# Performance work log

Measured on AMD Instinct MI355X. Metric: run time of the kernel, lower is better.

Reference implementation:

```python
import jax, jax.numpy as jnp
import numpy as np

D_MODEL = 1024
N_HEADS = 16
HEAD_DIM = D_MODEL // N_HEADS
ROPE_BASE = 10000.0


def setup_inputs() -> dict:
    key = jax.random.key(0)
    ks = jax.random.split(key, 9)
    s = 0.02
    inp = {
        "x": jax.random.normal(ks[0], (2, 2048, D_MODEL), dtype=jnp.float32),
        "Wq": jax.random.normal(ks[1], (D_MODEL, D_MODEL), dtype=jnp.float32) * s,
        "bq": jnp.zeros((D_MODEL,), dtype=jnp.float32),
        "Wk": jax.random.normal(ks[2], (D_MODEL, D_MODEL), dtype=jnp.float32) * s,
        "bk": jnp.zeros((D_MODEL,), dtype=jnp.float32),
        "Wv": jax.random.normal(ks[3], (D_MODEL, D_MODEL), dtype=jnp.float32) * s,
        "bv": jnp.zeros((D_MODEL,), dtype=jnp.float32),
        "Wo": jax.random.normal(ks[4], (D_MODEL, D_MODEL), dtype=jnp.float32) * s,
        "bo": jnp.zeros((D_MODEL,), dtype=jnp.float32),
    }
    return inp


def _rope_cos_sin(T, head_dim, dtype):
    inv_freq = 1.0 / (ROPE_BASE ** (jnp.arange(0, head_dim, 2, dtype=jnp.float32) / head_dim))
    pos = jnp.arange(T, dtype=jnp.float32)
    freqs = jnp.outer(pos, inv_freq)              # [T, head_dim/2]
    emb = jnp.concatenate([freqs, freqs], axis=-1)  # [T, head_dim]
    return jnp.cos(emb).astype(dtype), jnp.sin(emb).astype(dtype)


def _rotate_half(x):
    x1, x2 = jnp.split(x, 2, axis=-1)
    return jnp.concatenate([-x2, x1], axis=-1)


def reference(x, Wq, bq, Wk, bk, Wv, bv, Wo, bo):
    B, T, _ = x.shape
    H, Dh = N_HEADS, HEAD_DIM
    # projections (torch Linear: x @ W.T + b)
    q = (x @ Wq.T + bq).reshape(B, T, H, Dh).transpose(0, 2, 1, 3)  # [B,H,T,Dh]
    k = (x @ Wk.T + bk).reshape(B, T, H, Dh).transpose(0, 2, 1, 3)
    v = (x @ Wv.T + bv).reshape(B, T, H, Dh).transpose(0, 2, 1, 3)
    cos, sin = _rope_cos_sin(T, Dh, x.dtype)  # [T, Dh]
    cos = cos[None, None]
    sin = sin[None, None]
    q = q * cos + _rotate_half(q) * sin
    k = k * cos + _rotate_half(k) * sin
    scale = 1.0 / jnp.sqrt(jnp.asarray(Dh, dtype=x.dtype))
    attn = jnp.einsum("bhqd,bhkd->bhqk", q, k) * scale
    attn = jax.nn.softmax(attn, axis=-1)
    out = jnp.einsum("bhqk,bhkd->bhqd", attn, v)  # [B,H,T,Dh]
    out = out.transpose(0, 2, 1, 3).reshape(B, T, H * Dh)
    return out @ Wo.T + bo
```

## Files before the change

### kernel.cpp

```cpp
#include <hip/hip_runtime.h>
#include <hip/hip_bf16.h>
#include <cstdint>

#define D_MODEL 1024
#define NHEADS 16
#define HDIM 64
#define SEQ 2048
#define NBATCH 2
#define BT (NBATCH * SEQ)

typedef short bf16x8 __attribute__((ext_vector_type(8)));
typedef float f32x4 __attribute__((ext_vector_type(4)));
typedef unsigned short u16;

__device__ inline u16 f2bf(float f) {
    union { float f; unsigned int u; } x;
    x.f = f;
    unsigned int r = (x.u + 0x7fffu + ((x.u >> 16) & 1u)) >> 16;
    return (u16)r;
}

__device__ inline u16 f2bf_fast(float f) {
    union { float f; unsigned int u; } x;
    x.f = f;
    return (u16)((x.u + 0x8000u) >> 16);
}

__device__ inline void async_copy16(const u16* g, u16* l) {
    __builtin_amdgcn_global_load_lds((const __attribute__((address_space(1))) void*)g,
                                     (__attribute__((address_space(3))) void*)l, 16, 0, 0);
}

__global__ void cast_x_kernel(const float* __restrict__ src, u16* __restrict__ dst, int n4) {
    int i = blockIdx.x * blockDim.x + threadIdx.x;
    if (i >= n4) return;
    float4 v = ((const float4*)src)[i];
    ushort4 o;
    o.x = f2bf(v.x); o.y = f2bf(v.y); o.z = f2bf(v.z); o.w = f2bf(v.w);
    ((ushort4*)dst)[i] = o;
}

__global__ void cast_w_kernel(const float* __restrict__ wq, const float* __restrict__ wk,
                              const float* __restrict__ wv, const float* __restrict__ wo,
                              u16* __restrict__ dq, u16* __restrict__ dk,
                              u16* __restrict__ dv, u16* __restrict__ dow) {
    int z = blockIdx.z;
    const float* s = (z == 0) ? wq : (z == 1) ? wk : (z == 2) ? wv : wo;
    u16* d = (z == 0) ? dq : (z == 1) ? dk : (z == 2) ? dv : dow;
    int i = blockIdx.x * blockDim.x + threadIdx.x;
    float4 v = ((const float4*)s)[i];
    ushort4 o;
    o.x = f2bf(v.x); o.y = f2bf(v.y); o.z = f2bf(v.z); o.w = f2bf(v.w);
    ((ushort4*)d)[i] = o;
}

__global__ void rope_table_kernel(float* __restrict__ cosT, float* __restrict__ sinT) {
    int t = blockIdx.x;
    int d = threadIdx.x;
    float invf = expf(-(float)(d & 31) * (9.210340371976184f / 32.0f));
    float ang = (float)t * invf;
    float s, c;
    sincosf(ang, &s, &c);
    cosT[t * HDIM + d] = c;
    sinT[t * HDIM + d] = s;
}

__device__ inline void gemm_tile_core(const u16* __restrict__ A, const u16* __restrict__ Bw,
                                      int blkM, int blkN,
                                      u16* Asmem, u16* Bsmem, f32x4 acc[4][4]) {
    const int tid = threadIdx.x;
    const int lane = tid & 63;
    const int wave = tid >> 6;
    const int waveM = wave >> 1, waveN = wave & 1;
    const int quad = lane >> 4, l16 = lane & 15;

    const int srow = tid >> 2;
    const int scol = (tid & 3) << 3;
    const u16* Ag0 = A + (size_t)(blkM * 128 + srow) * D_MODEL + scol;
    const u16* Ag1 = Ag0 + (size_t)64 * D_MODEL;
    const u16* Bg0 = Bw + (size_t)(blkN * 128 + srow) * D_MODEL + scol;
    const u16* Bg1 = Bg0 + (size_t)64 * D_MODEL;
    u16* Al0 = Asmem + srow * 32 + scol;
    u16* Al1 = Al0 + 64 * 32;
    u16* Bl0 = Bsmem + srow * 32 + scol;
    u16* Bl1 = Bl0 + 64 * 32;

    for (int k0 = 0; k0 < D_MODEL; k0 += 32) {
        __syncthreads();
        async_copy16(Ag0 + k0, Al0);
        async_copy16(Ag1 + k0, Al1);
        async_copy16(Bg0 + k0, Bl0);
        async_copy16(Bg1 + k0, Bl1);
        __syncthreads();
        bf16x8 af[4], bfr[4];
#pragma unroll
        for (int mt = 0; mt < 4; ++mt)
            af[mt] = *(const bf16x8*)&Asmem[(waveM * 64 + mt * 16 + l16) * 32 + quad * 8];
#pragma unroll
        for (int nt = 0; nt < 4; ++nt)
            bfr[nt] = *(const bf16x8*)&Bsmem[(waveN * 64 + nt * 16 + l16) * 32 + quad * 8];
#pragma unroll
        for (int mt = 0; mt < 4; ++mt)
#pragma unroll
            for (int nt = 0; nt < 4; ++nt)
                acc[mt][nt] = __builtin_amdgcn_mfma_f32_16x16x32_bf16(af[mt], bfr[nt], acc[mt][nt], 0, 0, 0);
    }
}

#define QSCALE 0.1803368801111204f

__global__ __launch_bounds__(256) void gemm_qkv_kernel(
    const u16* __restrict__ xb,
    const u16* __restrict__ wqb, const u16* __restrict__ wkb, const u16* __restrict__ wvb,
    const float* __restrict__ bq, const float* __restrict__ bk, const float* __restrict__ bv,
    const float* __restrict__ cosT, const float* __restrict__ sinT,
    u16* __restrict__ Qb, u16* __restrict__ Kb, u16* __restrict__ VTb) {
    __shared__ __align__(16) u16 Asmem[128 * 32];
    __shared__ __align__(16) u16 Bsmem[128 * 32];
    const int z = blockIdx.z;
    const u16* Bw = (z == 0) ? wqb : (z == 1) ? wkb : wvb;
    const float* bias = (z == 0) ? bq : (z == 1) ? bk : bv;

    f32x4 acc[4][4];
#pragma unroll
    for (int mt = 0; mt < 4; ++mt)
#pragma unroll
        for (int nt = 0; nt < 4; ++nt)
            acc[mt][nt] = (f32x4){0.f, 0.f, 0.f, 0.f};

    gemm_tile_core(xb, Bw, blockIdx.x, blockIdx.y, Asmem, Bsmem, acc);

    const int lane = threadIdx.x & 63, wave = threadIdx.x >> 6;
    const int waveM = wave >> 1, waveN = wave & 1;
    const int quad = lane >> 4, l16 = lane & 15;
    const int gm0 = blockIdx.x * 128 + waveM * 64 + quad * 4;
    const int gn0 = blockIdx.y * 128 + waveN * 64 + l16;

    float bvv[4];
#pragma unroll
    for (int nt = 0; nt < 4; ++nt) bvv[nt] = bias[gn0 + nt * 16];
#pragma unroll
    for (int mt = 0; mt < 4; ++mt)
#pragma unroll
        for (int nt = 0; nt < 4; ++nt)
#pragma unroll
            for (int r = 0; r < 4; ++r) acc[mt][nt][r] += bvv[nt];

    if (z < 2) {
        u16* dst = (z == 0) ? Qb : Kb;
        const float post = (z == 0) ? QSCALE : 1.0f;
#pragma unroll
        for (int mt = 0; mt < 4; ++mt) {
#pragma unroll
            for (int nt = 0; nt < 4; ++nt) {
                int n = gn0 + nt * 16;
                int d = n & 63, h = n >> 6;
#pragma unroll
                for (int r = 0; r < 4; ++r) {
                    int gm = gm0 + mt * 16 + r;
                    int t = gm & (SEQ - 1), b = gm >> 11;
                    float c = cosT[t * HDIM + d], s = sinT[t * HDIM + d];
                    float part = acc[mt][nt ^ 2][r];
                    float rot = (d < 32) ? -part : part;
                    float val = (acc[mt][nt][r] * c + rot * s) * post;
                    dst[((b * NHEADS + h) * SEQ + t) * HDIM + d] = f2bf(val);
                }
            }
        }
    } else {
#pragma unroll
        for (int mt = 0; mt < 4; ++mt) {
#pragma unroll
            for (int nt = 0; nt < 4; ++nt) {
                int n = gn0 + nt * 16;
                int d = n & 63, h = n >> 6;
#pragma unroll
                for (int r = 0; r < 4; ++r) {
                    int gm = gm0 + mt * 16 + r;
                    int t = gm & (SEQ - 1), b = gm >> 11;
                    VTb[((b * NHEADS + h) * HDIM + d) * SEQ + t] = f2bf(acc[mt][nt][r]);
                }
            }
        }
    }
}

#define LPAD 72

__global__ __launch_bounds__(256) void flash_kernel(
    const u16* __restrict__ Qb, const u16* __restrict__ Kb, const u16* __restrict__ VTb,
    u16* __restrict__ attn) {
    __shared__ __align__(16) u16 Ks[64 * LPAD];
    __shared__ __align__(16) u16 VTs[64 * LPAD];
    __shared__ __align__(16) u16 Ps[4][16 * LPAD];

    const int tid = threadIdx.x;
    const int wave = tid >> 6, lane = tid & 63;
    const int quad = lane >> 4, l16 = lane & 15;
    const int bh = blockIdx.y;
    const u16* Qh = Qb + (size_t)bh * SEQ * HDIM;
    const u16* Kh = Kb + (size_t)bh * SEQ * HDIM;
    const u16* Vh = VTb + (size_t)bh * HDIM * SEQ;
    const int qbase = blockIdx.x * 64 + wave * 16;

    bf16x8 aq[2];
#pragma unroll
    for (int ks = 0; ks < 2; ++ks)
        aq[ks] = *(const bf16x8*)&Qh[(qbase + l16) * HDIM + ks * 32 + quad * 8];

    f32x4 o[4];
    float lsum[4] = {0.f, 0.f, 0.f, 0.f};
#pragma unroll
    for (int nt = 0; nt < 4; ++nt) o[nt] = (f32x4){0.f, 0.f, 0.f, 0.f};

    const int lr = tid >> 3, lc = (tid & 7) * 8;

    for (int kt = 0; kt < SEQ / 64; ++kt) {
        __syncthreads();
        *(int4*)&Ks[lr * LPAD + lc] = *(const int4*)&Kh[(kt * 64 + lr) * HDIM + lc];
        *(int4*)&Ks[(lr + 32) * LPAD + lc] = *(const int4*)&Kh[(kt * 64 + lr + 32) * HDIM + lc];
        *(int4*)&VTs[lr * LPAD + lc] = *(const int4*)&Vh[lr * SEQ + kt * 64 + lc];
        *(int4*)&VTs[(lr + 32) * LPAD + lc] = *(const int4*)&Vh[(lr + 32) * SEQ + kt * 64 + lc];
        __syncthreads();

        f32x4 sacc[4];
#pragma unroll
        for (int nt = 0; nt < 4; ++nt) sacc[nt] = (f32x4){0.f, 0.f, 0.f, 0.f};
#pragma unroll
        for (int ks = 0; ks < 2; ++ks) {
            bf16x8 bk_[4];
#pragma unroll
            for (int nt = 0; nt < 4; ++nt)
                bk_[nt] = *(const bf16x8*)&Ks[(nt * 16 + l16) * LPAD + ks * 32 + quad * 8];
#pragma unroll
            for (int nt = 0; nt < 4; ++nt)
                sacc[nt] = __builtin_amdgcn_mfma_f32_16x16x32_bf16(aq[ks], bk_[nt], sacc[nt], 0, 0, 0);
        }

#pragma unroll
        for (int nt = 0; nt < 4; ++nt) {
#pragma unroll
            for (int r = 0; r < 4; ++r) {
                float p = __builtin_amdgcn_exp2f(fminf(sacc[nt][r], 60.0f));
                lsum[r] += p;
                Ps[wave][(quad * 4 + r) * LPAD + nt * 16 + l16] = f2bf_fast(p);
            }
        }

#pragma unroll
        for (int ks = 0; ks < 2; ++ks) {
            bf16x8 ap, bv_[4];
            ap = *(const bf16x8*)&Ps[wave][l16 * LPAD + ks * 32 + quad * 8];
#pragma unroll
            for (int nt = 0; nt < 4; ++nt)
                bv_[nt] = *(const bf16x8*)&VTs[(nt * 16 + l16) * LPAD + ks * 32 + quad * 8];
#pragma unroll
            for (int nt = 0; nt < 4; ++nt)
                o[nt] = __builtin_amdgcn_mfma_f32_16x16x32_bf16(ap, bv_[nt], o[nt], 0, 0, 0);
        }
    }

#pragma unroll
    for (int off = 1; off < 16; off <<= 1)
#pragma unroll
        for (int r = 0; r < 4; ++r)
            lsum[r] += __shfl_xor(lsum[r], off, 64);

    const int b = bh >> 4, h = bh & 15;
    float rinv[4];
#pragma unroll
    for (int r = 0; r < 4; ++r) rinv[r] = 1.0f / lsum[r];
#pragma unroll
    for (int nt = 0; nt < 4; ++nt) {
        int d = nt * 16 + l16;
#pragma unroll
        for (int r = 0; r < 4; ++r) {
            int q = qbase + quad * 4 + r;
            attn[((size_t)(b * SEQ + q)) * D_MODEL + h * HDIM + d] = f2bf(o[nt][r] * rinv[r]);
        }
    }
}

__global__ __launch_bounds__(256) void gemm_out_kernel(
    const u16* __restrict__ attn, const u16* __restrict__ wob,
    const float* __restrict__ bo, float* __restrict__ dout) {
    __shared__ __align__(16) u16 Asmem[128 * 32];
    __shared__ __align__(16) u16 Bsmem[128 * 32];

    f32x4 acc[4][4];
#pragma unroll
    for (int mt = 0; mt < 4; ++mt)
#pragma unroll
        for (int nt = 0; nt < 4; ++nt) acc[mt][nt] = (f32x4){0.f, 0.f, 0.f, 0.f};

    gemm_tile_core(attn, wob, blockIdx.x, blockIdx.y, Asmem, Bsmem, acc);

    const int lane = threadIdx.x & 63, wave = threadIdx.x >> 6;
    const int waveM = wave >> 1, waveN = wave & 1;
    const int quad = lane >> 4, l16 = lane & 15;
    const int gm0 = blockIdx.x * 128 + waveM * 64 + quad * 4;
    const int gn0 = blockIdx.y * 128 + waveN * 64 + l16;

    float bvv[4];
#pragma unroll
    for (int nt = 0; nt < 4; ++nt) bvv[nt] = bo[gn0 + nt * 16];
#pragma unroll
    for (int mt = 0; mt < 4; ++mt)
#pragma unroll
        for (int nt = 0; nt < 4; ++nt)
#pragma unroll
            for (int r = 0; r < 4; ++r)
                dout[(size_t)(gm0 + mt * 16 + r) * D_MODEL + gn0 + nt * 16] = acc[mt][nt][r] + bvv[nt];
}

extern "C" void kernel_launch(void* const* d_in, const int* in_sizes, int n_in,
                              void* d_out, int out_size, void* d_ws, size_t ws_size,
                              hipStream_t stream) {
    const float* x  = (const float*)d_in[0];
    const float* Wq = (const float*)d_in[1];
    const float* bq = (const float*)d_in[2];
    const float* Wk = (const float*)d_in[3];
    const float* bk = (const float*)d_in[4];
    const float* Wv = (const float*)d_in[5];
    const float* bv = (const float*)d_in[6];
    const float* Wo = (const float*)d_in[7];
    const float* bo = (const float*)d_in[8];
    float* dout = (float*)d_out;

    char* ws = (char*)d_ws;
    size_t off = 0;
    u16* xb  = (u16*)(ws + off); off += (size_t)BT * D_MODEL * 2;
    u16* wqb = (u16*)(ws + off); off += (size_t)D_MODEL * D_MODEL * 2;
    u16* wkb = (u16*)(ws + off); off += (size_t)D_MODEL * D_MODEL * 2;
    u16* wvb = (u16*)(ws + off); off += (size_t)D_MODEL * D_MODEL * 2;
    u16* wob = (u16*)(ws + off); off += (size_t)D_MODEL * D_MODEL * 2;
    u16* Qb  = (u16*)(ws + off); off += (size_t)BT * D_MODEL * 2;
    u16* Kb  = (u16*)(ws + off); off += (size_t)BT * D_MODEL * 2;
    u16* VTb = (u16*)(ws + off); off += (size_t)BT * D_MODEL * 2;
    u16* attn = (u16*)(ws + off); off += (size_t)BT * D_MODEL * 2;
    float* cosT = (float*)(ws + off); off += (size_t)SEQ * HDIM * 4;
    float* sinT = (float*)(ws + off); off += (size_t)SEQ * HDIM * 4;

    cast_x_kernel<<<dim3((BT * D_MODEL / 4 + 255) / 256), 256, 0, stream>>>(x, xb, BT * D_MODEL / 4);
    cast_w_kernel<<<dim3(D_MODEL * D_MODEL / 4 / 256, 1, 4), 256, 0, stream>>>(Wq, Wk, Wv, Wo, wqb, wkb, wvb, wob);
    rope_table_kernel<<<dim3(SEQ), dim3(HDIM), 0, stream>>>(cosT, sinT);
    gemm_qkv_kernel<<<dim3(BT / 128, D_MODEL / 128, 3), 256, 0, stream>>>(
        xb, wqb, wkb, wvb, bq, bk, bv, cosT, sinT, Qb, Kb, VTb);
    flash_kernel<<<dim3(SEQ / 64, NBATCH * NHEADS), 256, 0, stream>>>(Qb, Kb, VTb, attn);
    gemm_out_kernel<<<dim3(BT / 128, D_MODEL / 128), 256, 0, stream>>>(attn, wob, bo, dout);
}
```

Measured before the change: 242.8 us.

## Double queries per wave in flash attention, fuse prep kernels, vectorize V^T stores

The flash kernel now handles 128 queries per block, with 32 per wave, so each K/V tile loaded into LDS is reused across twice as many queries. S is computed transposed (K as the A operand), which lets P be written to LDS as packed 8-byte stores and shrinks the row-sum reduction. The three preprocessing kernels (casts and RoPE table) are merged into one launch, and the RoPE table computes each half once and writes it to both halves. The V^T epilogue in the QKV GEMM writes four packed bf16 values per store instead of scalar stores. In exchange the flash grid has half as many blocks, and register pressure per wave rises.

```diff
diff --git a/kernel.cpp b/kernel.cpp
--- a/kernel.cpp
+++ b/kernel.cpp
@@ -12,18 +12,19 @@
 typedef short bf16x8 __attribute__((ext_vector_type(8)));
 typedef float f32x4 __attribute__((ext_vector_type(4)));
 typedef unsigned short u16;
+typedef unsigned int u32;
 
 __device__ inline u16 f2bf(float f) {
-    union { float f; unsigned int u; } x;
+    union { float f; u32 u; } x;
     x.f = f;
-    unsigned int r = (x.u + 0x7fffu + ((x.u >> 16) & 1u)) >> 16;
+    u32 r = (x.u + 0x7fffu + ((x.u >> 16) & 1u)) >> 16;
     return (u16)r;
 }
 
-__device__ inline u16 f2bf_fast(float f) {
-    union { float f; unsigned int u; } x;
-    x.f = f;
-    return (u16)((x.u + 0x8000u) >> 16);
+__device__ inline u32 pack2bf(float a, float b) {
+    union { float f; u32 u; } x, y;
+    x.f = a; y.f = b;
+    return ((x.u + 0x8000u) >> 16) | ((y.u + 0x8000u) & 0xffff0000u);
 }
 
 __device__ inline void async_copy16(const u16* g, u16* l) {
@@ -31,38 +32,44 @@
                                      (__attribute__((address_space(3))) void*)l, 16, 0, 0);
 }
 
-__global__ void cast_x_kernel(const float* __restrict__ src, u16* __restrict__ dst, int n4) {
-    int i = blockIdx.x * blockDim.x + threadIdx.x;
-    if (i >= n4) return;
-    float4 v = ((const float4*)src)[i];
-    ushort4 o;
-    o.x = f2bf(v.x); o.y = f2bf(v.y); o.z = f2bf(v.z); o.w = f2bf(v.w);
-    ((ushort4*)dst)[i] = o;
-}
-
-__global__ void cast_w_kernel(const float* __restrict__ wq, const float* __restrict__ wk,
-                              const float* __restrict__ wv, const float* __restrict__ wo,
-                              u16* __restrict__ dq, u16* __restrict__ dk,
-                              u16* __restrict__ dv, u16* __restrict__ dow) {
-    int z = blockIdx.z;
-    const float* s = (z == 0) ? wq : (z == 1) ? wk : (z == 2) ? wv : wo;
-    u16* d = (z == 0) ? dq : (z == 1) ? dk : (z == 2) ? dv : dow;
-    int i = blockIdx.x * blockDim.x + threadIdx.x;
-    float4 v = ((const float4*)s)[i];
-    ushort4 o;
-    o.x = f2bf(v.x); o.y = f2bf(v.y); o.z = f2bf(v.z); o.w = f2bf(v.w);
-    ((ushort4*)d)[i] = o;
-}
-
-__global__ void rope_table_kernel(float* __restrict__ cosT, float* __restrict__ sinT) {
-    int t = blockIdx.x;
-    int d = threadIdx.x;
-    float invf = expf(-(float)(d & 31) * (9.210340371976184f / 32.0f));
-    float ang = (float)t * invf;
-    float s, c;
-    sincosf(ang, &s, &c);
-    cosT[t * HDIM + d] = c;
-    sinT[t * HDIM + d] = s;
+#define X4 (BT * D_MODEL / 4)
+#define W4 (D_MODEL * D_MODEL / 4)
+#define ROPE_N (SEQ * 32)
+
+__global__ void prep_kernel(const float* __restrict__ x,
+                            const float* __restrict__ wq, const float* __restrict__ wk,
+                            const float* __restrict__ wv, const float* __restrict__ wo,
+                            u16* __restrict__ xb,
+                            u16* __restrict__ dq, u16* __restrict__ dk,
+                            u16* __restrict__ dv, u16* __restrict__ dow,
+                            float* __restrict__ cosT, float* __restrict__ sinT) {
+    int idx = blockIdx.x * blockDim.x + threadIdx.x;
+    if (idx < X4) {
+        float4 v = ((const float4*)x)[idx];
+        ushort4 o;
+        o.x = f2bf(v.x); o.y = f2bf(v.y); o.z = f2bf(v.z); o.w = f2bf(v.w);
+        ((ushort4*)xb)[idx] = o;
+    } else if (idx < X4 + 4 * W4) {
+        int j = idx - X4;
+        int w = j >> 18, i = j & (W4 - 1);
+        const float* s = (w == 0) ? wq : (w == 1) ? wk : (w == 2) ? wv : wo;
+        u16* d = (w == 0) ? dq : (w == 1) ? dk : (w == 2) ? dv : dow;
+        float4 v = ((const float4*)s)[i];
+        ushort4 o;
+        o.x = f2bf(v.x); o.y = f2bf(v.y); o.z = f2bf(v.z); o.w = f2bf(v.w);
+        ((ushort4*)d)[i] = o;
+    } else {
+        int j = idx - (X4 + 4 * W4);
+        if (j < ROPE_N) {
+            int t = j >> 5, dd = j & 31;
+            float invf = exp2f(-(float)dd * (13.287712379549449f / 32.0f));
+            float ang = (float)t * invf;
+            float s, c;
+            sincosf(ang, &s, &c);
+            cosT[t * HDIM + dd] = c;      cosT[t * HDIM + dd + 32] = c;
+            sinT[t * HDIM + dd] = s;      sinT[t * HDIM + dd + 32] = s;
+        }
+    }
 }
 
 __device__ inline void gemm_tile_core(const u16* __restrict__ A, const u16* __restrict__ Bw,
@@ -170,16 +177,16 @@
     } else {
 #pragma unroll
         for (int mt = 0; mt < 4; ++mt) {
+            int gm = gm0 + mt * 16;
+            int t0 = gm & (SEQ - 1), b = gm >> 11;
 #pragma unroll
             for (int nt = 0; nt < 4; ++nt) {
                 int n = gn0 + nt * 16;
                 int d = n & 63, h = n >> 6;
-#pragma unroll
-                for (int r = 0; r < 4; ++r) {
-                    int gm = gm0 + mt * 16 + r;
-                    int t = gm & (SEQ - 1), b = gm >> 11;
-                    VTb[((b * NHEADS + h) * HDIM + d) * SEQ + t] = f2bf(acc[mt][nt][r]);
-                }
+                uint2 w;
+                w.x = pack2bf(acc[mt][nt][0], acc[mt][nt][1]);
+                w.y = pack2bf(acc[mt][nt][2], acc[mt][nt][3]);
+                *(uint2*)&VTb[((size_t)(b * NHEADS + h) * HDIM + d) * SEQ + t0] = w;
             }
         }
     }
@@ -192,7 +199,7 @@
     u16* __restrict__ attn) {
     __shared__ __align__(16) u16 Ks[64 * LPAD];
     __shared__ __align__(16) u16 VTs[64 * LPAD];
-    __shared__ __align__(16) u16 Ps[4][16 * LPAD];
+    __shared__ __align__(16) u16 Ps[4][32 * LPAD];
 
     const int tid = threadIdx.x;
     const int wave = tid >> 6, lane = tid & 63;
@@ -201,82 +208,108 @@
     const u16* Qh = Qb + (size_t)bh * SEQ * HDIM;
     const u16* Kh = Kb + (size_t)bh * SEQ * HDIM;
     const u16* Vh = VTb + (size_t)bh * HDIM * SEQ;
-    const int qbase = blockIdx.x * 64 + wave * 16;
-
-    bf16x8 aq[2];
-#pragma unroll
-    for (int ks = 0; ks < 2; ++ks)
-        aq[ks] = *(const bf16x8*)&Qh[(qbase + l16) * HDIM + ks * 32 + quad * 8];
-
-    f32x4 o[4];
-    float lsum[4] = {0.f, 0.f, 0.f, 0.f};
-#pragma unroll
-    for (int nt = 0; nt < 4; ++nt) o[nt] = (f32x4){0.f, 0.f, 0.f, 0.f};
-
-    const int lr = tid >> 3, lc = (tid & 7) * 8;
+    const int qblk = blockIdx.x * 128 + wave * 32;
+    u16* Pw = (u16*)Ps[wave];
+
+    bf16x8 aq[2][2];
+#pragma unroll
+    for (int nt2 = 0; nt2 < 2; ++nt2)
+#pragma unroll
+        for (int ks = 0; ks < 2; ++ks)
+            aq[nt2][ks] = *(const bf16x8*)&Qh[(qblk + nt2 * 16 + l16) * HDIM + ks * 32 + quad * 8];
+
+    f32x4 o[2][4];
+    float lsum[2] = {0.f, 0.f};
+#pragma unroll
+    for (int mt2 = 0; mt2 < 2; ++mt2)
+#pragma unroll
+        for (int nt = 0; nt < 4; ++nt) o[mt2][nt] = (f32x4){0.f, 0.f, 0.f, 0.f};
+
+    const int lr = tid >> 2;
+    const int lc = (tid & 3) * 16;
 
     for (int kt = 0; kt < SEQ / 64; ++kt) {
         __syncthreads();
         *(int4*)&Ks[lr * LPAD + lc] = *(const int4*)&Kh[(kt * 64 + lr) * HDIM + lc];
-        *(int4*)&Ks[(lr + 32) * LPAD + lc] = *(const int4*)&Kh[(kt * 64 + lr + 32) * HDIM + lc];
+        *(int4*)&Ks[lr * LPAD + lc + 8] = *(const int4*)&Kh[(kt * 64 + lr) * HDIM + lc + 8];
         *(int4*)&VTs[lr * LPAD + lc] = *(const int4*)&Vh[lr * SEQ + kt * 64 + lc];
-        *(int4*)&VTs[(lr + 32) * LPAD + lc] = *(const int4*)&Vh[(lr + 32) * SEQ + kt * 64 + lc];
+        *(int4*)&VTs[lr * LPAD + lc + 8] = *(const int4*)&Vh[lr * SEQ + kt * 64 + lc + 8];
         __syncthreads();
 
-        f32x4 sacc[4];
-#pragma unroll
-        for (int nt = 0; nt < 4; ++nt) sacc[nt] = (f32x4){0.f, 0.f, 0.f, 0.f};
+        f32x4 sacc[4][2];
+#pragma unroll
+        for (int mt = 0; mt < 4; ++mt)
+#pragma unroll
+            for (int nt2 = 0; nt2 < 2; ++nt2) sacc[mt][nt2] = (f32x4){0.f, 0.f, 0.f, 0.f};
 #pragma unroll
         for (int ks = 0; ks < 2; ++ks) {
-            bf16x8 bk_[4];
+            bf16x8 kf[4];
+#pragma unroll
+            for (int mt = 0; mt < 4; ++mt)
+                kf[mt] = *(const bf16x8*)&Ks[(mt * 16 + l16) * LPAD + ks * 32 + quad * 8];
+#pragma unroll
+            for (int mt = 0; mt < 4; ++mt)
+#pragma unroll
+                for (int nt2 = 0; nt2 < 2; ++nt2)
+                    sacc[mt][nt2] = __builtin_amdgcn_mfma_f32_16x16x32_bf16(kf[mt], aq[nt2][ks], sacc[mt][nt2], 0, 0, 0);
+        }
+
+#pragma unroll
+        for (int mt = 0; mt < 4; ++mt) {
+#pragma unroll
+            for (int nt2 = 0; nt2 < 2; ++nt2) {
+                float p0 = __builtin_amdgcn_exp2f(fminf(sacc[mt][nt2][0], 60.0f));
+                float p1 = __builtin_amdgcn_exp2f(fminf(sacc[mt][nt2][1], 60.0f));
+                float p2 = __builtin_amdgcn_exp2f(fminf(sacc[mt][nt2][2], 60.0f));
+                float p3 = __builtin_amdgcn_exp2f(fminf(sacc[mt][nt2][3], 60.0f));
+                lsum[nt2] += (p0 + p1) + (p2 + p3);
+                uint2 w;
+                w.x = pack2bf(p0, p1);
+                w.y = pack2bf(p2, p3);
+                *(uint2*)&Pw[(nt2 * 16 + l16) * LPAD + mt * 16 + quad * 4] = w;
+            }
+        }
+
+#pragma unroll
+        for (int ks = 0; ks < 2; ++ks) {
+            bf16x8 pf[2], vf[4];
+#pragma unroll
+            for (int mt2 = 0; mt2 < 2; ++mt2)
+                pf[mt2] = *(const bf16x8*)&Pw[(mt2 * 16 + l16) * LPAD + ks * 32 + quad * 8];
 #pragma unroll
             for (int nt = 0; nt < 4; ++nt)
-                bk_[nt] = *(const bf16x8*)&Ks[(nt * 16 + l16) * LPAD + ks * 32 + quad * 8];
-#pragma unroll
-            for (int nt = 0; nt < 4; ++nt)
-                sacc[nt] = __builtin_amdgcn_mfma_f32_16x16x32_bf16(aq[ks], bk_[nt], sacc[nt], 0, 0, 0);
-        }
-
+                vf[nt] = *(const bf16x8*)&VTs[(nt * 16 + l16) * LPAD + ks * 32 + quad * 8];
+#pragma unroll
+            for (int mt2 = 0; mt2 < 2; ++mt2)
+#pragma unroll
+                for (int nt = 0; nt < 4; ++nt)
+                    o[mt2][nt] = __builtin_amdgcn_mfma_f32_16x16x32_bf16(pf[mt2], vf[nt], o[mt2][nt], 0, 0, 0);
+        }
+    }
+
+#pragma unroll
+    for (int nt2 = 0; nt2 < 2; ++nt2) {
+        lsum[nt2] += __shfl_xor(lsum[nt2], 16, 64);
+        lsum[nt2] += __shfl_xor(lsum[nt2], 32, 64);
+    }
+    float rinv[2][4];
+#pragma unroll
+    for (int mt2 = 0; mt2 < 2; ++mt2)
+#pragma unroll
+        for (int r = 0; r < 4; ++r)
+            rinv[mt2][r] = 1.0f / __shfl(lsum[mt2], quad * 4 + r, 64);
+
+    const int b = bh >> 4, h = bh & 15;
+#pragma unroll
+    for (int mt2 = 0; mt2 < 2; ++mt2) {
 #pragma unroll
         for (int nt = 0; nt < 4; ++nt) {
+            int d = nt * 16 + l16;
 #pragma unroll
             for (int r = 0; r < 4; ++r) {
-                float p = __builtin_amdgcn_exp2f(fminf(sacc[nt][r], 60.0f));
-                lsum[r] += p;
-                Ps[wave][(quad * 4 + r) * LPAD + nt * 16 + l16] = f2bf_fast(p);
+                int q = qblk + mt2 * 16 + quad * 4 + r;
+                attn[((size_t)(b * SEQ + q)) * D_MODEL + h * HDIM + d] = f2bf(o[mt2][nt][r] * rinv[mt2][r]);
             }
-        }
-
-#pragma unroll
-        for (int ks = 0; ks < 2; ++ks) {
-            bf16x8 ap, bv_[4];
-            ap = *(const bf16x8*)&Ps[wave][l16 * LPAD + ks * 32 + quad * 8];
-#pragma unroll
-            for (int nt = 0; nt < 4; ++nt)
-                bv_[nt] = *(const bf16x8*)&VTs[(nt * 16 + l16) * LPAD + ks * 32 + quad * 8];
-#pragma unroll
-            for (int nt = 0; nt < 4; ++nt)
-                o[nt] = __builtin_amdgcn_mfma_f32_16x16x32_bf16(ap, bv_[nt], o[nt], 0, 0, 0);
-        }
-    }
-
-#pragma unroll
-    for (int off = 1; off < 16; off <<= 1)
-#pragma unroll
-        for (int r = 0; r < 4; ++r)
-            lsum[r] += __shfl_xor(lsum[r], off, 64);
-
-    const int b = bh >> 4, h = bh & 15;
-    float rinv[4];
-#pragma unroll
-    for (int r = 0; r < 4; ++r) rinv[r] = 1.0f / lsum[r];
-#pragma unroll
-    for (int nt = 0; nt < 4; ++nt) {
-        int d = nt * 16 + l16;
-#pragma unroll
-        for (int r = 0; r < 4; ++r) {
-            int q = qbase + quad * 4 + r;
-            attn[((size_t)(b * SEQ + q)) * D_MODEL + h * HDIM + d] = f2bf(o[nt][r] * rinv[r]);
         }
     }
 }
@@ -341,11 +374,11 @@
     float* cosT = (float*)(ws + off); off += (size_t)SEQ * HDIM * 4;
     float* sinT = (float*)(ws + off); off += (size_t)SEQ * HDIM * 4;
 
-    cast_x_kernel<<<dim3((BT * D_MODEL / 4 + 255) / 256), 256, 0, stream>>>(x, xb, BT * D_MODEL / 4);
-    cast_w_kernel<<<dim3(D_MODEL * D_MODEL / 4 / 256, 1, 4), 256, 0, stream>>>(Wq, Wk, Wv, Wo, wqb, wkb, wvb, wob);
-    rope_table_kernel<<<dim3(SEQ), dim3(HDIM), 0, stream>>>(cosT, sinT);
+    const int prepN = X4 + 4 * W4 + ROPE_N;
+    prep_kernel<<<dim3((prepN + 255) / 256), 256, 0, stream>>>(
+        x, Wq, Wk, Wv, Wo, xb, wqb, wkb, wvb, wob, cosT, sinT);
     gemm_qkv_kernel<<<dim3(BT / 128, D_MODEL / 128, 3), 256, 0, stream>>>(
         xb, wqb, wkb, wvb, bq, bk, bv, cosT, sinT, Qb, Kb, VTb);
-    flash_kernel<<<dim3(SEQ / 64, NBATCH * NHEADS), 256, 0, stream>>>(Qb, Kb, VTb, attn);
+    flash_kernel<<<dim3(SEQ / 128, NBATCH * NHEADS), 256, 0, stream>>>(Qb, Kb, VTb, attn);
     gemm_out_kernel<<<dim3(BT / 128, D_MODEL / 128), 256, 0, stream>>>(attn, wob, bo, dout);
 }
```

After: 229.6 us. 1.06x faster.
